# Optimization experiments

Measured on AMD Instinct MI355X. Metric: run time of the kernel, lower is better.

Reference implementation:

```python
import jax, jax.numpy as jnp
import numpy as np

N_EMBD = 768
HEAD_SIZE = 64
BLOCK_SIZE = 64

def setup_inputs() -> dict:
    key = jax.random.key(0)
    kx, kk, kq, kv = jax.random.split(key, 4)
    B, T = 2048, BLOCK_SIZE
    scale = 1.0 / np.sqrt(N_EMBD)
    x = jax.random.normal(kx, (B, T, N_EMBD), dtype=jnp.float32)
    # torch Linear(no bias): y = x @ W.T with W [out,in]; store as [in,out]
    Wk = jax.random.normal(kk, (N_EMBD, HEAD_SIZE), dtype=jnp.float32) * scale
    Wq = jax.random.normal(kq, (N_EMBD, HEAD_SIZE), dtype=jnp.float32) * scale
    Wv = jax.random.normal(kv, (N_EMBD, HEAD_SIZE), dtype=jnp.float32) * scale
    return {"x": x, "Wk": Wk, "Wq": Wq, "Wv": Wv}

def reference(x, Wk, Wq, Wv):
    B, T, C = x.shape
    k = jnp.einsum('btc,ch->bth', x, Wk)  # [B,T,H]
    q = jnp.einsum('btc,ch->bth', x, Wq)
    v = jnp.einsum('btc,ch->bth', x, Wv)
    scale = k.shape[-1] ** -0.5
    wei = jnp.einsum('bth,bsh->bts', q, k) * scale  # [B,T,T]
    causal = jnp.tril(jnp.ones((T, T), dtype=bool))
    wei = jnp.where(causal, wei, -jnp.inf)
    wei = jax.nn.softmax(wei, axis=-1)  # dropout p=0.0 is identity
    out = jnp.einsum('bts,bsh->bth', wei, v)  # [B,T,H]
    return out
```

## Files before the change

kernel.cpp:

```cpp
#include <hip/hip_runtime.h>


#define BATCHES 2048
#define SEQ 64
#define CDIM 768
#define HDIM 64
#define NCX 24

typedef __bf16 bf16x8 __attribute__((ext_vector_type(8)));
typedef float f32x4v __attribute__((ext_vector_type(4)));
typedef unsigned short u16x8 __attribute__((ext_vector_type(8)));

__device__ __forceinline__ unsigned short f2bf(float f) {
  return __builtin_bit_cast(unsigned short, (__bf16)f);
}

__device__ __forceinline__ int swz(int row, int col) {
  return row * 64 + (col ^ ((row & 7) << 3));
}

__device__ __forceinline__ f32x4v mfma16(bf16x8 a, bf16x8 b, f32x4v c) {
  return __builtin_amdgcn_mfma_f32_16x16x32_bf16(a, b, c, 0, 0, 0);
}

__device__ __forceinline__ bf16x8 lds_frag(const unsigned short* p, int row, int col) {
  return __builtin_bit_cast(bf16x8, *reinterpret_cast<const u16x8*>(p + swz(row, col)));
}

__device__ __forceinline__ void gl_lds16(const void* g, void* l) {
  __builtin_amdgcn_global_load_lds(
      (const __attribute__((address_space(1))) void*)g,
      (__attribute__((address_space(3))) void*)l, 16, 0, 0);
}

__global__ __launch_bounds__(256) void prep_wt_kernel(
    const float* __restrict__ Wk, const float* __restrict__ Wq,
    const float* __restrict__ Wv, unsigned short* __restrict__ wt) {
  int i = blockIdx.x * 256 + threadIdx.x;
  if (i >= 3 * HDIM * CDIM) return;
  int c = i / 6144;
  int r2 = i - c * 6144;
  int slot = r2 >> 3;
  int e = r2 & 7;
  int row = slot >> 2;
  int p = slot & 3;
  int g = p ^ ((row >> 1) & 3);
  int k = c * 32 + g * 8 + e;
  int mat = row >> 6;
  int h = row & 63;
  const float* W = (mat == 0) ? Wq : ((mat == 1) ? Wk : Wv);
  wt[i] = f2bf(W[k * HDIM + h]);
}

__global__ __launch_bounds__(512, 2) void head_fused_kernel(
    const float* __restrict__ x, const unsigned short* __restrict__ wt,
    float* __restrict__ out) {
  const int bid = blockIdx.x;
  const int tid = threadIdx.x;
  const int w = tid >> 6;
  const int ww = w & 3;
  const int bat = w >> 2;
  const int lane = tid & 63;
  const int lane15 = lane & 15;
  const int lhi = lane >> 4;

  __shared__ __align__(16) unsigned char smem[49152];

  const char* wbaseA = (const char*)wt + (w * 64 + lane) * 16;
  const char* wbase2 = (const char*)wt + (((8 + w) * 64 + lane)) * 16;
  const int wdstA = (w * 64 + lane) * 16;
  const int wdst2 = ((8 + w) * 64 + lane) * 16;

  #define STAGE_WT(cn, B)                                                   \
    do {                                                                    \
      char* wbp = (char*)smem + (B) * 12288;                                \
      gl_lds16(wbaseA + (cn) * 12288, wbp + wdstA);                         \
      if (w < 4) gl_lds16(wbase2 + (cn) * 12288, wbp + wdst2);              \
    } while (0)

  const char* xlane = (const char*)x + (size_t)(2 * bid + bat) * 196608 +
                      (16 * ww + lane15) * 3072 + lhi * 32;
  #define ISSUE_X(cn, D0, D1)                                               \
    do {                                                                    \
      D0 = *reinterpret_cast<const f32x4v*>(xlane + (cn) * 128);            \
      D1 = *reinterpret_cast<const f32x4v*>(xlane + (cn) * 128 + 16);       \
    } while (0)

  const f32x4v z4 = {0.f, 0.f, 0.f, 0.f};
  f32x4v accq[4], acck[4], accv[4];
  #pragma unroll
  for (int n = 0; n < 4; ++n) { accq[n] = z4; acck[n] = z4; accv[n] = z4; }

  #define COMPUTE(c, X0, X1)                                                \
    do {                                                                    \
      const unsigned short* ws =                                            \
          (const unsigned short*)((char*)smem + ((c) & 1) * 12288);         \
      u16x8 ar;                                                             \
      _Pragma("unroll")                                                     \
      for (int i = 0; i < 4; ++i) { ar[i] = f2bf(X0[i]); ar[4 + i] = f2bf(X1[i]); } \
      bf16x8 a = __builtin_bit_cast(bf16x8, ar);                            \
      _Pragma("unroll")                                                     \
      for (int n = 0; n < 4; ++n) {                                         \
        int brq = 0 * HDIM + 16 * n + lane15;                               \
        int bpq = lhi ^ ((brq >> 1) & 3);                                   \
        bf16x8 bq = __builtin_bit_cast(bf16x8,                              \
            *reinterpret_cast<const u16x8*>(ws + brq * 32 + bpq * 8));      \
        accq[n] = mfma16(a, bq, accq[n]);                                   \
        int brk = 1 * HDIM + 16 * n + lane15;                               \
        int bpk = lhi ^ ((brk >> 1) & 3);                                   \
        bf16x8 bk = __builtin_bit_cast(bf16x8,                              \
            *reinterpret_cast<const u16x8*>(ws + brk * 32 + bpk * 8));      \
        acck[n] = mfma16(a, bk, acck[n]);                                   \
        int brv = 2 * HDIM + 16 * n + lane15;                               \
        int bpv = lhi ^ ((brv >> 1) & 3);                                   \
        bf16x8 bv = __builtin_bit_cast(bf16x8,                              \
            *reinterpret_cast<const u16x8*>(ws + brv * 32 + bpv * 8));      \
        accv[n] = mfma16(a, bv, accv[n]);                                   \
      }                                                                     \
    } while (0)

  #define ITER(c, X0, X1)                                                   \
    do {                                                                    \
      if ((c) < NCX - 1) {                                                  \
        if (w < 4) asm volatile("s_waitcnt vmcnt(4)" ::: "memory");         \
        else       asm volatile("s_waitcnt vmcnt(3)" ::: "memory");         \
      } else {                                                              \
        asm volatile("s_waitcnt vmcnt(0)" ::: "memory");                    \
      }                                                                     \
      __builtin_amdgcn_sched_barrier(0);                                    \
      __builtin_amdgcn_s_barrier();                                         \
      COMPUTE(c, X0, X1);                                                   \
      asm volatile("s_waitcnt lgkmcnt(0)" ::: "memory");                    \
      __builtin_amdgcn_sched_barrier(0);                                    \
      __builtin_amdgcn_s_barrier();                                         \
      if ((c) + 2 < NCX) {                                                  \
        STAGE_WT((c) + 2, (c) & 1);                                         \
        __builtin_amdgcn_sched_barrier(0);                                  \
        ISSUE_X((c) + 2, X0, X1);                                           \
        __builtin_amdgcn_sched_barrier(0);                                  \
      }                                                                     \
    } while (0)

  f32x4v PA0, PA1, PB0, PB1;

  STAGE_WT(0, 0);
  __builtin_amdgcn_sched_barrier(0);
  ISSUE_X(0, PA0, PA1);
  __builtin_amdgcn_sched_barrier(0);
  STAGE_WT(1, 1);
  __builtin_amdgcn_sched_barrier(0);
  ISSUE_X(1, PB0, PB1);
  __builtin_amdgcn_sched_barrier(0);

  ITER(0, PA0, PA1);   ITER(1, PB0, PB1);
  ITER(2, PA0, PA1);   ITER(3, PB0, PB1);
  ITER(4, PA0, PA1);   ITER(5, PB0, PB1);
  ITER(6, PA0, PA1);   ITER(7, PB0, PB1);
  ITER(8, PA0, PA1);   ITER(9, PB0, PB1);
  ITER(10, PA0, PA1);  ITER(11, PB0, PB1);
  ITER(12, PA0, PA1);  ITER(13, PB0, PB1);
  ITER(14, PA0, PA1);  ITER(15, PB0, PB1);
  ITER(16, PA0, PA1);  ITER(17, PB0, PB1);
  ITER(18, PA0, PA1);  ITER(19, PB0, PB1);
  ITER(20, PA0, PA1);  ITER(21, PB0, PB1);
  ITER(22, PA0, PA1);  ITER(23, PB0, PB1);

  #undef ITER
  #undef COMPUTE
  #undef ISSUE_X
  #undef STAGE_WT

  unsigned short* k_lds  = (unsigned short*)((char*)smem + bat * 24576);
  unsigned short* vT_lds = (unsigned short*)((char*)smem + bat * 24576 + 8192);
  unsigned short* qp_lds = (unsigned short*)((char*)smem + bat * 24576 + 16384);

  #pragma unroll
  for (int n = 0; n < 4; ++n) {
    int h = 16 * n + lane15;
    #pragma unroll
    for (int j = 0; j < 4; ++j) {
      int s = 16 * ww + lhi * 4 + j;
      k_lds[swz(s, h)] = f2bf(acck[n][j]);
      vT_lds[swz(h, s)] = f2bf(accv[n][j]);
      qp_lds[swz(s, h)] = f2bf(accq[n][j]);
    }
  }
  __syncthreads();

  const int trow = 16 * ww + lane15;
  bf16x8 aq0 = lds_frag(qp_lds, trow, lhi * 8);
  bf16x8 aq1 = lds_frag(qp_lds, trow, 32 + lhi * 8);
  f32x4v accS[4];
  #pragma unroll
  for (int n = 0; n < 4; ++n) accS[n] = z4;
  #pragma unroll
  for (int sB = 0; sB < 4; ++sB) {
    if (sB <= ww) {
      bf16x8 bk0 = lds_frag(k_lds, 16 * sB + lane15, lhi * 8);
      bf16x8 bk1 = lds_frag(k_lds, 16 * sB + lane15, 32 + lhi * 8);
      accS[sB] = mfma16(aq0, bk0, accS[sB]);
      accS[sB] = mfma16(aq1, bk1, accS[sB]);
    }
  }

  float rinv[4];
  #pragma unroll
  for (int j = 0; j < 4; ++j) {
    int t = 16 * ww + lhi * 4 + j;
    float zv[4];
    float m = -3.0e38f;
    #pragma unroll
    for (int sB = 0; sB < 4; ++sB) {
      int sc = 16 * sB + lane15;
      float zz = (sB <= ww && sc <= t) ? accS[sB][j] * 0.125f : -3.0e38f;
      zv[sB] = zz;
      m = fmaxf(m, zz);
    }
    #pragma unroll
    for (int off = 1; off < 16; off <<= 1) m = fmaxf(m, __shfl_xor(m, off));
    float sum = 0.f;
    float pv[4];
    #pragma unroll
    for (int sB = 0; sB < 4; ++sB) {
      float pe = __expf(zv[sB] - m);
      pv[sB] = pe;
      sum += pe;
    }
    #pragma unroll
    for (int off = 1; off < 16; off <<= 1) sum += __shfl_xor(sum, off);
    rinv[j] = 1.0f / sum;
    #pragma unroll
    for (int sB = 0; sB < 4; ++sB)
      qp_lds[swz(t, 16 * sB + lane15)] = f2bf(pv[sB]);
  }
  __syncthreads();

  f32x4v accO[4];
  #pragma unroll
  for (int n = 0; n < 4; ++n) accO[n] = z4;
  #pragma unroll
  for (int s0 = 0; s0 < 64; s0 += 32) {
    if (s0 <= 16 * ww + 15) {
      bf16x8 ap = lds_frag(qp_lds, trow, s0 + lhi * 8);
      #pragma unroll
      for (int n = 0; n < 4; ++n) {
        bf16x8 bv = lds_frag(vT_lds, 16 * n + lane15, s0 + lhi * 8);
        accO[n] = mfma16(ap, bv, accO[n]);
      }
    }
  }

  float* op = out + (size_t)(2 * bid + bat) * (SEQ * HDIM);
  #pragma unroll
  for (int n = 0; n < 4; ++n) {
    int h = 16 * n + lane15;
    #pragma unroll
    for (int j = 0; j < 4; ++j) {
      int t = 16 * ww + lhi * 4 + j;
      op[t * HDIM + h] = accO[n][j] * rinv[j];
    }
  }
}

extern "C" void kernel_launch(void* const* d_in, const int* in_sizes, int n_in,
                              void* d_out, int out_size, void* d_ws, size_t ws_size,
                              hipStream_t stream) {
  const float* x  = (const float*)d_in[0];
  const float* Wk = (const float*)d_in[1];
  const float* Wq = (const float*)d_in[2];
  const float* Wv = (const float*)d_in[3];
  float* out = (float*)d_out;
  unsigned short* wt = (unsigned short*)d_ws;

  hipLaunchKernelGGL(prep_wt_kernel, dim3((3 * HDIM * CDIM + 255) / 256), dim3(256),
                     0, stream, Wk, Wq, Wv, wt);
  hipLaunchKernelGGL(head_fused_kernel, dim3(BATCHES / 2), dim3(512), 0, stream,
                     x, wt, out);
}
```

Baseline: 111.2 us.

## Stage half the projection weights into LDS per pass, dropping per-chunk barriers

Replaces the double-buffered per-chunk weight staging (two block barriers per K-chunk) with two passes. Each pass bulk-loads half of the bf16 weight matrix (144KB) into LDS, and x loads run four chunks deep, so the 12 chunks of a pass need no intra-pass barriers. This cuts synchronisation and keeps more loads in flight. In exchange LDS grows from 48KB to 144KB, so occupancy drops to one 512-thread block per CU, and each pass starts with a large exposed weight load.

```diff
diff --git a/kernel.cpp b/kernel.cpp
--- a/kernel.cpp
+++ b/kernel.cpp
@@ -5,7 +5,6 @@
 #define SEQ 64
 #define CDIM 768
 #define HDIM 64
-#define NCX 24
 
 typedef __bf16 bf16x8 __attribute__((ext_vector_type(8)));
 typedef float f32x4v __attribute__((ext_vector_type(4)));
@@ -52,7 +51,7 @@
   wt[i] = f2bf(W[k * HDIM + h]);
 }
 
-__global__ __launch_bounds__(512, 2) void head_fused_kernel(
+__global__ __launch_bounds__(512, 1) void head_fused_kernel(
     const float* __restrict__ x, const unsigned short* __restrict__ wt,
     float* __restrict__ out) {
   const int bid = blockIdx.x;
@@ -64,26 +63,24 @@
   const int lane15 = lane & 15;
   const int lhi = lane >> 4;
 
-  __shared__ __align__(16) unsigned char smem[49152];
-
-  const char* wbaseA = (const char*)wt + (w * 64 + lane) * 16;
-  const char* wbase2 = (const char*)wt + (((8 + w) * 64 + lane)) * 16;
-  const int wdstA = (w * 64 + lane) * 16;
-  const int wdst2 = ((8 + w) * 64 + lane) * 16;
-
-  #define STAGE_WT(cn, B)                                                   \
-    do {                                                                    \
-      char* wbp = (char*)smem + (B) * 12288;                                \
-      gl_lds16(wbaseA + (cn) * 12288, wbp + wdstA);                         \
-      if (w < 4) gl_lds16(wbase2 + (cn) * 12288, wbp + wdst2);              \
+  __shared__ __align__(16) unsigned char smem[147456];
+
+  #define STAGE_WT_HALF(p)                                                  \
+    do {                                                                    \
+      _Pragma("unroll")                                                     \
+      for (int k = 0; k < 18; ++k) {                                        \
+        int region = k * 8 + w;                                             \
+        gl_lds16((const char*)wt + (p) * 147456 + region * 1024 + lane * 16,\
+                 (char*)smem + region * 1024 + lane * 16);                  \
+      }                                                                     \
     } while (0)
 
   const char* xlane = (const char*)x + (size_t)(2 * bid + bat) * 196608 +
                       (16 * ww + lane15) * 3072 + lhi * 32;
-  #define ISSUE_X(cn, D0, D1)                                               \
-    do {                                                                    \
-      D0 = *reinterpret_cast<const f32x4v*>(xlane + (cn) * 128);            \
-      D1 = *reinterpret_cast<const f32x4v*>(xlane + (cn) * 128 + 16);       \
+  #define ISSUE_X(cg, D0, D1)                                               \
+    do {                                                                    \
+      D0 = *reinterpret_cast<const f32x4v*>(xlane + (cg) * 128);            \
+      D1 = *reinterpret_cast<const f32x4v*>(xlane + (cg) * 128 + 16);       \
     } while (0)
 
   const f32x4v z4 = {0.f, 0.f, 0.f, 0.f};
@@ -91,10 +88,10 @@
   #pragma unroll
   for (int n = 0; n < 4; ++n) { accq[n] = z4; acck[n] = z4; accv[n] = z4; }
 
-  #define COMPUTE(c, X0, X1)                                                \
+  #define COMPUTE(cl, X0, X1)                                               \
     do {                                                                    \
       const unsigned short* ws =                                            \
-          (const unsigned short*)((char*)smem + ((c) & 1) * 12288);         \
+          (const unsigned short*)((char*)smem + (cl) * 12288);              \
       u16x8 ar;                                                             \
       _Pragma("unroll")                                                     \
       for (int i = 0; i < 4; ++i) { ar[i] = f2bf(X0[i]); ar[4 + i] = f2bf(X1[i]); } \
@@ -119,56 +116,51 @@
       }                                                                     \
     } while (0)
 
-  #define ITER(c, X0, X1)                                                   \
-    do {                                                                    \
-      if ((c) < NCX - 1) {                                                  \
-        if (w < 4) asm volatile("s_waitcnt vmcnt(4)" ::: "memory");         \
-        else       asm volatile("s_waitcnt vmcnt(3)" ::: "memory");         \
-      } else {                                                              \
-        asm volatile("s_waitcnt vmcnt(0)" ::: "memory");                    \
-      }                                                                     \
-      __builtin_amdgcn_sched_barrier(0);                                    \
-      __builtin_amdgcn_s_barrier();                                         \
-      COMPUTE(c, X0, X1);                                                   \
+  #define ITER(p, cl, X0, X1)                                               \
+    do {                                                                    \
+      if ((cl) <= 8)       asm volatile("s_waitcnt vmcnt(6)" ::: "memory"); \
+      else if ((cl) == 9)  asm volatile("s_waitcnt vmcnt(4)" ::: "memory"); \
+      else if ((cl) == 10) asm volatile("s_waitcnt vmcnt(2)" ::: "memory"); \
+      else                 asm volatile("s_waitcnt vmcnt(0)" ::: "memory"); \
+      __builtin_amdgcn_sched_barrier(0);                                    \
+      COMPUTE(cl, X0, X1);                                                  \
+      if ((cl) + 4 < 12) ISSUE_X((p) * 12 + (cl) + 4, X0, X1);              \
+      __builtin_amdgcn_sched_barrier(0);                                    \
+    } while (0)
+
+  f32x4v PA0, PA1, PB0, PB1, PC0, PC1, PD0, PD1;
+
+  #define PASS(p)                                                           \
+    do {                                                                    \
+      STAGE_WT_HALF(p);                                                     \
+      __builtin_amdgcn_sched_barrier(0);                                    \
+      ISSUE_X((p) * 12 + 0, PA0, PA1);                                      \
+      ISSUE_X((p) * 12 + 1, PB0, PB1);                                      \
+      ISSUE_X((p) * 12 + 2, PC0, PC1);                                      \
+      ISSUE_X((p) * 12 + 3, PD0, PD1);                                      \
+      __builtin_amdgcn_sched_barrier(0);                                    \
+      asm volatile("s_waitcnt vmcnt(8)" ::: "memory");    \
+      __builtin_amdgcn_sched_barrier(0);                                    \
+      __builtin_amdgcn_s_barrier();       \
+      ITER(p, 0, PA0, PA1);  ITER(p, 1, PB0, PB1);                          \
+      ITER(p, 2, PC0, PC1);  ITER(p, 3, PD0, PD1);                          \
+      ITER(p, 4, PA0, PA1);  ITER(p, 5, PB0, PB1);                          \
+      ITER(p, 6, PC0, PC1);  ITER(p, 7, PD0, PD1);                          \
+      ITER(p, 8, PA0, PA1);  ITER(p, 9, PB0, PB1);                          \
+      ITER(p, 10, PC0, PC1); ITER(p, 11, PD0, PD1);                         \
       asm volatile("s_waitcnt lgkmcnt(0)" ::: "memory");                    \
       __builtin_amdgcn_sched_barrier(0);                                    \
-      __builtin_amdgcn_s_barrier();                                         \
-      if ((c) + 2 < NCX) {                                                  \
-        STAGE_WT((c) + 2, (c) & 1);                                         \
-        __builtin_amdgcn_sched_barrier(0);                                  \
-        ISSUE_X((c) + 2, X0, X1);                                           \
-        __builtin_amdgcn_sched_barrier(0);                                  \
-      }                                                                     \
-    } while (0)
-
-  f32x4v PA0, PA1, PB0, PB1;
-
-  STAGE_WT(0, 0);
-  __builtin_amdgcn_sched_barrier(0);
-  ISSUE_X(0, PA0, PA1);
-  __builtin_amdgcn_sched_barrier(0);
-  STAGE_WT(1, 1);
-  __builtin_amdgcn_sched_barrier(0);
-  ISSUE_X(1, PB0, PB1);
-  __builtin_amdgcn_sched_barrier(0);
-
-  ITER(0, PA0, PA1);   ITER(1, PB0, PB1);
-  ITER(2, PA0, PA1);   ITER(3, PB0, PB1);
-  ITER(4, PA0, PA1);   ITER(5, PB0, PB1);
-  ITER(6, PA0, PA1);   ITER(7, PB0, PB1);
-  ITER(8, PA0, PA1);   ITER(9, PB0, PB1);
-  ITER(10, PA0, PA1);  ITER(11, PB0, PB1);
-  ITER(12, PA0, PA1);  ITER(13, PB0, PB1);
-  ITER(14, PA0, PA1);  ITER(15, PB0, PB1);
-  ITER(16, PA0, PA1);  ITER(17, PB0, PB1);
-  ITER(18, PA0, PA1);  ITER(19, PB0, PB1);
-  ITER(20, PA0, PA1);  ITER(21, PB0, PB1);
-  ITER(22, PA0, PA1);  ITER(23, PB0, PB1);
-
+      __builtin_amdgcn_s_barrier();    \
+    } while (0)
+
+  PASS(0);
+  PASS(1);
+
+  #undef PASS
   #undef ITER
   #undef COMPUTE
   #undef ISSUE_X
-  #undef STAGE_WT
+  #undef STAGE_WT_HALF
 
   unsigned short* k_lds  = (unsigned short*)((char*)smem + bat * 24576);
   unsigned short* vT_lds = (unsigned short*)((char*)smem + bat * 24576 + 8192);
```

Result: slower. 114.1 us (+2.6%).

## Use one batch per 256-thread block and deepen x prefetch to three stages

Applied to the files above, without the earlier changes.

Each block now handles a single batch with 4 waves instead of two batches with 8 waves. The launch uses 2048 blocks, LDS per block is halved, and launch bounds allow 4 blocks per CU. The x register prefetch goes from two chunks ahead to three, with the vmcnt waits adjusted to match. Weight staging into LDS is now amortized over only one batch per block, which doubles the total weight traffic from L2.

```diff
diff --git a/kernel.cpp b/kernel.cpp
--- a/kernel.cpp
+++ b/kernel.cpp
@@ -52,34 +52,35 @@
   wt[i] = f2bf(W[k * HDIM + h]);
 }
 
-__global__ __launch_bounds__(512, 2) void head_fused_kernel(
+__global__ __launch_bounds__(256, 4) void head_fused_kernel(
     const float* __restrict__ x, const unsigned short* __restrict__ wt,
     float* __restrict__ out) {
   const int bid = blockIdx.x;
   const int tid = threadIdx.x;
   const int w = tid >> 6;
-  const int ww = w & 3;
-  const int bat = w >> 2;
   const int lane = tid & 63;
   const int lane15 = lane & 15;
   const int lhi = lane >> 4;
 
-  __shared__ __align__(16) unsigned char smem[49152];
-
-  const char* wbaseA = (const char*)wt + (w * 64 + lane) * 16;
-  const char* wbase2 = (const char*)wt + (((8 + w) * 64 + lane)) * 16;
-  const int wdstA = (w * 64 + lane) * 16;
-  const int wdst2 = ((8 + w) * 64 + lane) * 16;
+  __shared__ __align__(16) unsigned char smem[24576];
+
+  const char* wb0 = (const char*)wt + ((0 * 4 + w) * 64 + lane) * 16;
+  const char* wb1 = (const char*)wt + ((1 * 4 + w) * 64 + lane) * 16;
+  const char* wb2 = (const char*)wt + ((2 * 4 + w) * 64 + lane) * 16;
+  const int wd0 = ((0 * 4 + w) * 64 + lane) * 16;
+  const int wd1 = ((1 * 4 + w) * 64 + lane) * 16;
+  const int wd2 = ((2 * 4 + w) * 64 + lane) * 16;
 
   #define STAGE_WT(cn, B)                                                   \
     do {                                                                    \
       char* wbp = (char*)smem + (B) * 12288;                                \
-      gl_lds16(wbaseA + (cn) * 12288, wbp + wdstA);                         \
-      if (w < 4) gl_lds16(wbase2 + (cn) * 12288, wbp + wdst2);              \
-    } while (0)
-
-  const char* xlane = (const char*)x + (size_t)(2 * bid + bat) * 196608 +
-                      (16 * ww + lane15) * 3072 + lhi * 32;
+      gl_lds16(wb0 + (cn) * 12288, wbp + wd0);                              \
+      gl_lds16(wb1 + (cn) * 12288, wbp + wd1);                              \
+      gl_lds16(wb2 + (cn) * 12288, wbp + wd2);                              \
+    } while (0)
+
+  const char* xlane = (const char*)x + (size_t)bid * 196608 +
+                      (16 * w + lane15) * 3072 + lhi * 32;
   #define ISSUE_X(cn, D0, D1)                                               \
     do {                                                                    \
       D0 = *reinterpret_cast<const f32x4v*>(xlane + (cn) * 128);            \
@@ -121,27 +122,22 @@
 
   #define ITER(c, X0, X1)                                                   \
     do {                                                                    \
-      if ((c) < NCX - 1) {                                                  \
-        if (w < 4) asm volatile("s_waitcnt vmcnt(4)" ::: "memory");         \
-        else       asm volatile("s_waitcnt vmcnt(3)" ::: "memory");         \
-      } else {                                                              \
-        asm volatile("s_waitcnt vmcnt(0)" ::: "memory");                    \
-      }                                                                     \
+      if ((c) <= 21)      asm volatile("s_waitcnt vmcnt(7)" ::: "memory");  \
+      else if ((c) == 22) asm volatile("s_waitcnt vmcnt(5)" ::: "memory");  \
+      else                asm volatile("s_waitcnt vmcnt(0)" ::: "memory");  \
       __builtin_amdgcn_sched_barrier(0);                                    \
       __builtin_amdgcn_s_barrier();                                         \
       COMPUTE(c, X0, X1);                                                   \
       asm volatile("s_waitcnt lgkmcnt(0)" ::: "memory");                    \
       __builtin_amdgcn_sched_barrier(0);                                    \
       __builtin_amdgcn_s_barrier();                                         \
-      if ((c) + 2 < NCX) {                                                  \
-        STAGE_WT((c) + 2, (c) & 1);                                         \
-        __builtin_amdgcn_sched_barrier(0);                                  \
-        ISSUE_X((c) + 2, X0, X1);                                           \
-        __builtin_amdgcn_sched_barrier(0);                                  \
-      }                                                                     \
-    } while (0)
-
-  f32x4v PA0, PA1, PB0, PB1;
+      if ((c) + 2 < NCX) STAGE_WT((c) + 2, (c) & 1);                        \
+      __builtin_amdgcn_sched_barrier(0);                                    \
+      if ((c) + 3 < NCX) ISSUE_X((c) + 3, X0, X1);                          \
+      __builtin_amdgcn_sched_barrier(0);                                    \
+    } while (0)
+
+  f32x4v PA0, PA1, PB0, PB1, PC0, PC1;
 
   STAGE_WT(0, 0);
   __builtin_amdgcn_sched_barrier(0);
@@ -150,36 +146,33 @@
   STAGE_WT(1, 1);
   __builtin_amdgcn_sched_barrier(0);
   ISSUE_X(1, PB0, PB1);
-  __builtin_amdgcn_sched_barrier(0);
-
-  ITER(0, PA0, PA1);   ITER(1, PB0, PB1);
-  ITER(2, PA0, PA1);   ITER(3, PB0, PB1);
-  ITER(4, PA0, PA1);   ITER(5, PB0, PB1);
-  ITER(6, PA0, PA1);   ITER(7, PB0, PB1);
-  ITER(8, PA0, PA1);   ITER(9, PB0, PB1);
-  ITER(10, PA0, PA1);  ITER(11, PB0, PB1);
-  ITER(12, PA0, PA1);  ITER(13, PB0, PB1);
-  ITER(14, PA0, PA1);  ITER(15, PB0, PB1);
-  ITER(16, PA0, PA1);  ITER(17, PB0, PB1);
-  ITER(18, PA0, PA1);  ITER(19, PB0, PB1);
-  ITER(20, PA0, PA1);  ITER(21, PB0, PB1);
-  ITER(22, PA0, PA1);  ITER(23, PB0, PB1);
+  ISSUE_X(2, PC0, PC1);
+  __builtin_amdgcn_sched_barrier(0);
+
+  ITER(0, PA0, PA1);   ITER(1, PB0, PB1);   ITER(2, PC0, PC1);
+  ITER(3, PA0, PA1);   ITER(4, PB0, PB1);   ITER(5, PC0, PC1);
+  ITER(6, PA0, PA1);   ITER(7, PB0, PB1);   ITER(8, PC0, PC1);
+  ITER(9, PA0, PA1);   ITER(10, PB0, PB1);  ITER(11, PC0, PC1);
+  ITER(12, PA0, PA1);  ITER(13, PB0, PB1);  ITER(14, PC0, PC1);
+  ITER(15, PA0, PA1);  ITER(16, PB0, PB1);  ITER(17, PC0, PC1);
+  ITER(18, PA0, PA1);  ITER(19, PB0, PB1);  ITER(20, PC0, PC1);
+  ITER(21, PA0, PA1);  ITER(22, PB0, PB1);  ITER(23, PC0, PC1);
 
   #undef ITER
   #undef COMPUTE
   #undef ISSUE_X
   #undef STAGE_WT
 
-  unsigned short* k_lds  = (unsigned short*)((char*)smem + bat * 24576);
-  unsigned short* vT_lds = (unsigned short*)((char*)smem + bat * 24576 + 8192);
-  unsigned short* qp_lds = (unsigned short*)((char*)smem + bat * 24576 + 16384);
+  unsigned short* k_lds  = (unsigned short*)smem;
+  unsigned short* vT_lds = (unsigned short*)(smem + 8192);
+  unsigned short* qp_lds = (unsigned short*)(smem + 16384);
 
   #pragma unroll
   for (int n = 0; n < 4; ++n) {
     int h = 16 * n + lane15;
     #pragma unroll
     for (int j = 0; j < 4; ++j) {
-      int s = 16 * ww + lhi * 4 + j;
+      int s = 16 * w + lhi * 4 + j;
       k_lds[swz(s, h)] = f2bf(acck[n][j]);
       vT_lds[swz(h, s)] = f2bf(accv[n][j]);
       qp_lds[swz(s, h)] = f2bf(accq[n][j]);
@@ -187,7 +180,7 @@
   }
   __syncthreads();
 
-  const int trow = 16 * ww + lane15;
+  const int trow = 16 * w + lane15;
   bf16x8 aq0 = lds_frag(qp_lds, trow, lhi * 8);
   bf16x8 aq1 = lds_frag(qp_lds, trow, 32 + lhi * 8);
   f32x4v accS[4];
@@ -195,7 +188,7 @@
   for (int n = 0; n < 4; ++n) accS[n] = z4;
   #pragma unroll
   for (int sB = 0; sB < 4; ++sB) {
-    if (sB <= ww) {
+    if (sB <= w) {
       bf16x8 bk0 = lds_frag(k_lds, 16 * sB + lane15, lhi * 8);
       bf16x8 bk1 = lds_frag(k_lds, 16 * sB + lane15, 32 + lhi * 8);
       accS[sB] = mfma16(aq0, bk0, accS[sB]);
@@ -206,13 +199,13 @@
   float rinv[4];
   #pragma unroll
   for (int j = 0; j < 4; ++j) {
-    int t = 16 * ww + lhi * 4 + j;
+    int t = 16 * w + lhi * 4 + j;
     float zv[4];
     float m = -3.0e38f;
     #pragma unroll
     for (int sB = 0; sB < 4; ++sB) {
       int sc = 16 * sB + lane15;
-      float zz = (sB <= ww && sc <= t) ? accS[sB][j] * 0.125f : -3.0e38f;
+      float zz = (sB <= w && sc <= t) ? accS[sB][j] * 0.125f : -3.0e38f;
       zv[sB] = zz;
       m = fmaxf(m, zz);
     }
@@ -240,7 +233,7 @@
   for (int n = 0; n < 4; ++n) accO[n] = z4;
   #pragma unroll
   for (int s0 = 0; s0 < 64; s0 += 32) {
-    if (s0 <= 16 * ww + 15) {
+    if (s0 <= 16 * w + 15) {
       bf16x8 ap = lds_frag(qp_lds, trow, s0 + lhi * 8);
       #pragma unroll
       for (int n = 0; n < 4; ++n) {
@@ -250,13 +243,13 @@
     }
   }
 
-  float* op = out + (size_t)(2 * bid + bat) * (SEQ * HDIM);
+  float* op = out + (size_t)bid * (SEQ * HDIM);
   #pragma unroll
   for (int n = 0; n < 4; ++n) {
     int h = 16 * n + lane15;
     #pragma unroll
     for (int j = 0; j < 4; ++j) {
-      int t = 16 * ww + lhi * 4 + j;
+      int t = 16 * w + lhi * 4 + j;
       op[t * HDIM + h] = accO[n][j] * rinv[j];
     }
   }
@@ -274,6 +267,6 @@
 
   hipLaunchKernelGGL(prep_wt_kernel, dim3((3 * HDIM * CDIM + 255) / 256), dim3(256),
                      0, stream, Wk, Wq, Wv, wt);
-  hipLaunchKernelGGL(head_fused_kernel, dim3(BATCHES / 2), dim3(512), 0, stream,
+  hipLaunchKernelGGL(head_fused_kernel, dim3(BATCHES), dim3(256), 0, stream,
                      x, wt, out);
 }
```

Measured after the change: 124.0 us. 11.5% more time.
